# Optimization experiments

Measured on AMD Instinct MI355X. Metric: run time of the kernel, lower is better.

## Reference

```python
import jax, jax.numpy as jnp
import numpy as np

ETA = 1.0
BETA = 0.6
LN_EPS = 1e-5


def layer_norm(x, scale, bias):
    mu = x.mean(-1, keepdims=True)
    var = ((x - mu) ** 2).mean(-1, keepdims=True)
    return (x - mu) / jnp.sqrt(var + LN_EPS) * scale + bias


def setup_inputs() -> dict:
    B, N, S, C, D = 8, 2048, 16, 32, 128
    key = jax.random.key(0)
    ks = jax.random.split(key, 10)
    X_short = jax.random.normal(ks[0], (B, N, S, C), dtype=jnp.float32)
    # binary temporal validity mask (float, as multiplied in the original)
    mask_short = (jax.random.uniform(ks[1], (B, N, S)) > 0.3).astype(jnp.float32)
    A_stat = jax.random.uniform(ks[2], (N, N), dtype=jnp.float32)
    M_mask = jax.random.randint(ks[3], (N, N), 0, 2).astype(jnp.int32)
    M_mask = M_mask.at[jnp.arange(N), jnp.arange(N)].set(1)  # keep self-edges so no all-masked row
    node_reliab = jax.random.uniform(ks[4], (B, N), dtype=jnp.float32)
    # learned parameters (stored (in, out) so application is x @ W)
    W_proj = jax.random.normal(ks[5], (C, D), dtype=jnp.float32) / np.sqrt(C)
    Wq = jax.random.normal(ks[6], (D, D), dtype=jnp.float32) / np.sqrt(D)
    Wk = jax.random.normal(ks[7], (D, D), dtype=jnp.float32) / np.sqrt(D)
    W_lin = jax.random.normal(ks[8], (D, D), dtype=jnp.float32) / np.sqrt(D)
    ln1_scale = jnp.ones((D,), jnp.float32)
    ln1_bias = jnp.zeros((D,), jnp.float32)
    ln2_scale = jnp.ones((D,), jnp.float32)
    ln2_bias = jnp.zeros((D,), jnp.float32)
    return {
        "X_short": X_short, "mask_short": mask_short, "A_stat": A_stat,
        "M_mask": M_mask, "node_reliab": node_reliab,
        "W_proj": W_proj, "Wq": Wq, "Wk": Wk, "W_lin": W_lin,
        "ln1_scale": ln1_scale, "ln1_bias": ln1_bias,
        "ln2_scale": ln2_scale, "ln2_bias": ln2_bias,
    }


def reference(X_short, mask_short, A_stat, M_mask, node_reliab,
              W_proj, Wq, Wk, W_lin, ln1_scale, ln1_bias, ln2_scale, ln2_bias):
    D = W_proj.shape[1]
    # masked temporal mean pooling over S
    denom = jnp.maximum(mask_short.sum(axis=2, keepdims=True), 1.0)      # (B,N,1)
    x = (X_short * mask_short[..., None]).sum(axis=2) / denom            # (B,N,C)
    Hn = x @ W_proj                                                      # (B,N,D)
    # dynamic graph attention
    Q = Hn @ Wq
    K = Hn @ Wk
    logits = jnp.einsum('bnd,bmd->bnm', Q, K) / jnp.sqrt(jnp.float32(D))
    p = jnp.clip(A_stat, 1e-3, 1.0 - 1e-3)
    bias = jnp.log(p / (1.0 - p))                                        # logit
    logits = logits + ETA * bias[None]
    edge = (M_mask != 0)[None]                                           # (1,N,N)
    logits = jnp.where(edge, logits, -jnp.inf)
    Adyn = jax.nn.softmax(logits, axis=-1)                               # (B,N,N)
    # fuse with static adjacency, reliability scaling, mask, row-renormalize
    A_fuse = BETA * Adyn + (1.0 - BETA) * A_stat[None]
    r = jnp.clip(node_reliab, 0.0, 1.0)                                  # (B,N)
    A_fuse = A_fuse * r[:, :, None] * r[:, None, :]
    A_fuse = A_fuse * M_mask.astype(A_fuse.dtype)[None]
    A_fuse = A_fuse / (A_fuse.sum(axis=-1, keepdims=True) + 1e-8)
    # propagate: A @ H -> linear -> relu -> (dropout=eval identity) -> LN -> outer LN
    H = jnp.einsum('bnm,bmd->bnd', A_fuse, Hn)
    H = H @ W_lin
    H = layer_norm(jax.nn.relu(H), ln1_scale, ln1_bias)
    out = layer_norm(H, ln2_scale, ln2_bias)
    return out, A_fuse
```

## Files before the change

### kernel.cpp

```cpp
#include <hip/hip_runtime.h>
#include <math.h>

#define BB 8
#define NN 2048
#define SS 16
#define CC 32
#define DD 128

typedef unsigned short u16;
typedef __attribute__((ext_vector_type(8))) short bf16x8;
typedef __attribute__((ext_vector_type(4))) float f32x4;

__device__ inline u16 f2bf(float f) {
    union { float f; unsigned u; } c; c.f = f;
    unsigned r = c.u + 0x7fff + ((c.u >> 16) & 1);
    return (u16)(r >> 16);
}
__device__ inline float bf2f(u16 h) {
    union { unsigned u; float f; } c; c.u = ((unsigned)h) << 16;
    return c.f;
}
__device__ inline u16 f2h(float f) {
    union { _Float16 h; u16 u; } c; c.h = (_Float16)f;
    return c.u;
}
__device__ inline float h2f(u16 u) {
    union { _Float16 h; u16 v; } c; c.v = u;
    return (float)c.h;
}
__device__ inline float clamp01(float v) { return fminf(fmaxf(v, 0.f), 1.f); }

__global__ __launch_bounds__(256) void wcomb_kernel(const float* __restrict__ Wproj,
                                                    const float* __restrict__ Wq,
                                                    const float* __restrict__ Wk,
                                                    float* __restrict__ Wpq,
                                                    float* __restrict__ Wpk) {
    int g = blockIdx.x * 256 + threadIdx.x;
    int d = g & 127;
    int c = (g >> 7) & 31;
    int mat = g >> 12;
    const float* Wt = mat ? Wk : Wq;
    float acc = 0.f;
#pragma unroll 4
    for (int e = 0; e < DD; ++e)
        acc = fmaf(Wproj[c * DD + e], Wt[e * DD + d], acc);
    (mat ? Wpk : Wpq)[c * DD + d] = acc;
}

__global__ __launch_bounds__(256) void wlt_kernel(const float* __restrict__ Wl,
                                                  u16* __restrict__ WlT) {
    int g = blockIdx.x * 256 + threadIdx.x;
    int dp = g >> 7, d = g & 127;
    WlT[dp * DD + d] = f2bf(Wl[d * DD + dp]);
}

__global__ __launch_bounds__(256) void bias_prep_kernel(const float* __restrict__ Astat,
                                                        const int* __restrict__ Mm,
                                                        u16* __restrict__ lgh,
                                                        u16* __restrict__ am) {
    size_t g = ((size_t)blockIdx.x * 256 + threadIdx.x) * 4;
    float4 a4 = *(const float4*)&Astat[g];
    int4 m4 = *(const int4*)&Mm[g];
    float a[4] = {a4.x, a4.y, a4.z, a4.w};
    int mm[4] = {m4.x, m4.y, m4.z, m4.w};
    ushort4 lo, ao;
    u16 lg[4], ab[4];
#pragma unroll
    for (int j = 0; j < 4; ++j) {
        float p = fminf(fmaxf(a[j], 1e-3f), 1.f - 1e-3f);
        float l = __logf(p / (1.f - p));
        lg[j] = mm[j] ? f2h(l) : (u16)0xFC00;
        ab[j] = mm[j] ? f2bf(a[j]) : (u16)0;
    }
    lo.x = lg[0]; lo.y = lg[1]; lo.z = lg[2]; lo.w = lg[3];
    ao.x = ab[0]; ao.y = ab[1]; ao.z = ab[2]; ao.w = ab[3];
    *(ushort4*)&lgh[g] = lo;
    *(ushort4*)&am[g] = ao;
}

__global__ __launch_bounds__(256) void proj3_kernel(const float* __restrict__ X,
                                                    const float* __restrict__ Msk,
                                                    const float* __restrict__ Wproj,
                                                    const float* __restrict__ Wpq,
                                                    const float* __restrict__ Wpk,
                                                    u16* __restrict__ HnT,
                                                    u16* __restrict__ Qb,
                                                    u16* __restrict__ Kb) {
    __shared__ float wp[CC * DD], wq[CC * DD], wk[CC * DD];
    __shared__ float xs[CC * 36];
    int t = threadIdx.x;
    for (int i = t; i < CC * DD; i += 256) {
        wp[i] = Wproj[i];
        wq[i] = Wpq[i];
        wk[i] = Wpk[i];
    }
    int rbase = blockIdx.x * 32;
    {
        int row = t >> 3, cg = t & 7;
        const float* xrow = X + ((size_t)(rbase + row) * SS) * CC + cg * 4;
        const float* mrow = Msk + (size_t)(rbase + row) * SS;
        float4 acc = make_float4(0.f, 0.f, 0.f, 0.f);
        float msum = 0.f;
#pragma unroll
        for (int s = 0; s < SS; ++s) {
            float mv = mrow[s];
            float4 xv = *(const float4*)&xrow[s * CC];
            msum += mv;
            acc.x = fmaf(xv.x, mv, acc.x);
            acc.y = fmaf(xv.y, mv, acc.y);
            acc.z = fmaf(xv.z, mv, acc.z);
            acc.w = fmaf(xv.w, mv, acc.w);
        }
        float inv = 1.f / fmaxf(msum, 1.0f);
        xs[(cg * 4 + 0) * 36 + row] = acc.x * inv;
        xs[(cg * 4 + 1) * 36 + row] = acc.y * inv;
        xs[(cg * 4 + 2) * 36 + row] = acc.z * inv;
        xs[(cg * 4 + 3) * 36 + row] = acc.w * inv;
    }
    __syncthreads();

    int col = t & 127;
    int g = t >> 7;
    float ah[16], aq[16], ak[16];
#pragma unroll
    for (int i = 0; i < 16; ++i) { ah[i] = 0.f; aq[i] = 0.f; ak[i] = 0.f; }

#pragma unroll 4
    for (int k = 0; k < CC; ++k) {
        float wpv = wp[k * DD + col], wqv = wq[k * DD + col], wkv = wk[k * DD + col];
        const float4* xp = (const float4*)&xs[k * 36 + g * 16];
        float4 a0 = xp[0], a1 = xp[1], a2 = xp[2], a3 = xp[3];
        float xv[16] = {a0.x, a0.y, a0.z, a0.w, a1.x, a1.y, a1.z, a1.w,
                        a2.x, a2.y, a2.z, a2.w, a3.x, a3.y, a3.z, a3.w};
#pragma unroll
        for (int i = 0; i < 16; ++i) {
            ah[i] = fmaf(xv[i], wpv, ah[i]);
            aq[i] = fmaf(xv[i], wqv, aq[i]);
            ak[i] = fmaf(xv[i], wkv, ak[i]);
        }
    }
    const float scale = 0.08838834764831845f;
#pragma unroll
    for (int i = 0; i < 16; ++i) {
        size_t row = (size_t)(rbase + g * 16 + i);
        Qb[row * DD + col] = f2bf(aq[i] * scale);
        Kb[row * DD + col] = f2bf(ak[i]);
    }
    int b = rbase >> 11;
    int n0 = (rbase & (NN - 1)) + g * 16;
    u16* hp = HnT + (size_t)b * DD * NN + (size_t)col * NN + n0;
    unsigned pk[8];
#pragma unroll
    for (int i = 0; i < 8; ++i)
        pk[i] = (unsigned)f2bf(ah[2 * i]) | ((unsigned)f2bf(ah[2 * i + 1]) << 16);
    *(uint4*)&hp[0] = make_uint4(pk[0], pk[1], pk[2], pk[3]);
    *(uint4*)&hp[8] = make_uint4(pk[4], pk[5], pk[6], pk[7]);
}

#define LQT 136
__global__ __launch_bounds__(256) void stats_kernel(
        const u16* __restrict__ Qb, const u16* __restrict__ Kb,
        const u16* __restrict__ lgh, const u16* __restrict__ am,
        const float* __restrict__ rel,
        u16* __restrict__ Ebuf, float* __restrict__ part) {
    __shared__ u16 Qs[32 * LQT];
    __shared__ u16 Ks[128 * LQT];
    __shared__ float redE[128], redR[128], redA[128];
    int cs = blockIdx.x, rt = blockIdx.y, b = blockIdx.z;
    int R0 = rt * 32, C0 = cs * 512;
    int t = threadIdx.x;
    int lane = t & 63, w = t >> 6, q = lane >> 4, r16 = lane & 15;

    const u16* Qg = Qb + ((size_t)b * NN + R0) * DD;
#pragma unroll
    for (int rep = 0; rep < 2; ++rep) {
        int e = rep * 256 + t;
        int row = e >> 4, seg = e & 15;
        *(uint4*)&Qs[row * LQT + seg * 8] = *(const uint4*)&Qg[row * DD + seg * 8];
    }
    const u16* Kg = Kb + (size_t)b * NN * DD;
    float ER[2][4], LR[2][4], LA[2][4];
#pragma unroll
    for (int i = 0; i < 2; ++i)
#pragma unroll
        for (int r = 0; r < 4; ++r) { ER[i][r] = 0.f; LR[i][r] = 0.f; LA[i][r] = 0.f; }

    for (int ct = 0; ct < 4; ++ct) {
        __syncthreads();
#pragma unroll
        for (int rep = 0; rep < 8; ++rep) {
            int e = rep * 256 + t;
            int colr = e >> 4, seg = e & 15;
            *(uint4*)&Ks[colr * LQT + seg * 8] =
                *(const uint4*)&Kg[(size_t)(C0 + ct * 128 + colr) * DD + seg * 8];
        }
        __syncthreads();
        f32x4 acc[2][2];
#pragma unroll
        for (int i = 0; i < 2; ++i)
#pragma unroll
            for (int j = 0; j < 2; ++j)
                acc[i][j] = (f32x4){0.f, 0.f, 0.f, 0.f};
#pragma unroll
        for (int ksp = 0; ksp < 4; ++ksp) {
            int ko = ksp * 32 + q * 8;
            bf16x8 a0 = *(const bf16x8*)&Qs[r16 * LQT + ko];
            bf16x8 a1 = *(const bf16x8*)&Qs[(16 + r16) * LQT + ko];
            bf16x8 b0 = *(const bf16x8*)&Ks[(w * 32 + r16) * LQT + ko];
            bf16x8 b1 = *(const bf16x8*)&Ks[(w * 32 + 16 + r16) * LQT + ko];
            acc[0][0] = __builtin_amdgcn_mfma_f32_16x16x32_bf16(a0, b0, acc[0][0], 0, 0, 0);
            acc[0][1] = __builtin_amdgcn_mfma_f32_16x16x32_bf16(a0, b1, acc[0][1], 0, 0, 0);
            acc[1][0] = __builtin_amdgcn_mfma_f32_16x16x32_bf16(a1, b0, acc[1][0], 0, 0, 0);
            acc[1][1] = __builtin_amdgcn_mfma_f32_16x16x32_bf16(a1, b1, acc[1][1], 0, 0, 0);
        }
        int m0 = C0 + ct * 128 + w * 32;
        float rm0 = clamp01(rel[b * NN + m0 + r16]);
        float rm1 = clamp01(rel[b * NN + m0 + 16 + r16]);
#pragma unroll
        for (int i = 0; i < 2; ++i)
#pragma unroll
            for (int r = 0; r < 4; ++r) {
                int n = R0 + i * 16 + q * 4 + r;
                const u16* lrow = lgh + (size_t)n * NN + m0;
                const u16* arow = am + (size_t)n * NN + m0;
                float lg0 = h2f(lrow[r16]), lg1 = h2f(lrow[16 + r16]);
                float a0 = bf2f(arow[r16]), a1 = bf2f(arow[16 + r16]);
                u16 eb0 = f2bf(__expf(acc[i][0][r] + lg0));
                u16 eb1 = f2bf(__expf(acc[i][1][r] + lg1));
                size_t o = ((size_t)b * NN + n) * NN + m0;
                Ebuf[o + r16] = eb0;
                Ebuf[o + 16 + r16] = eb1;
                float e0 = bf2f(eb0), e1 = bf2f(eb1);
                ER[i][r] += e0 + e1;
                LR[i][r] = fmaf(e0, rm0, fmaf(e1, rm1, LR[i][r]));
                LA[i][r] = fmaf(a0, rm0, fmaf(a1, rm1, LA[i][r]));
            }
    }
#pragma unroll
    for (int i = 0; i < 2; ++i)
#pragma unroll
        for (int r = 0; r < 4; ++r) {
            float e = ER[i][r], lr = LR[i][r], la = LA[i][r];
#pragma unroll
            for (int off = 1; off < 16; off <<= 1) {
                e += __shfl_xor(e, off);
                lr += __shfl_xor(lr, off);
                la += __shfl_xor(la, off);
            }
            if (r16 == 0) {
                int row = i * 16 + q * 4 + r;
                redE[w * 32 + row] = e;
                redR[w * 32 + row] = lr;
                redA[w * 32 + row] = la;
            }
        }
    __syncthreads();
    if (t < 32) {
        float es = redE[t] + redE[32 + t] + redE[64 + t] + redE[96 + t];
        float lr = redR[t] + redR[32 + t] + redR[64 + t] + redR[96 + t];
        float la = redA[t] + redA[32 + t] + redA[64 + t] + redA[96 + t];
        float* p = part + ((size_t)((b * 64 + rt) * 4 + cs)) * 96;
        p[t] = es;
        p[32 + t] = lr;
        p[64 + t] = la;
    }
}

#define LPT 72
#define LWT 136
__global__ __launch_bounds__(256) void prop_kernel(
        const u16* __restrict__ Ebuf, const u16* __restrict__ am,
        const float* __restrict__ part, const float* __restrict__ rel,
        const u16* __restrict__ HnT, const u16* __restrict__ WlT,
        const float* __restrict__ s1, const float* __restrict__ b1,
        const float* __restrict__ s2, const float* __restrict__ b2,
        float* __restrict__ Af, float* __restrict__ out) {
    __shared__ union {
        struct { u16 As[32 * LPT]; u16 Bs[128 * LPT]; } ab;
        struct { u16 Ws[128 * LWT]; u16 Hs[32 * LWT]; } fin;
    } sm;
    __shared__ float redS[128], redQ[128];
    __shared__ float2 MV[32];
    __shared__ float2 cfs[32];
    int rt = blockIdx.x, b = blockIdx.y;
    int R0 = rt * 32;
    int t = threadIdx.x;
    int lane = t & 63, w = t >> 6, q = lane >> 4, r16 = lane & 15;
    int srow = t >> 3, sseg = t & 7;

    if (t < 32) {
        const float* p = part + ((size_t)((b * 64 + rt) * 4)) * 96;
        float es = 0.f, lr = 0.f, la = 0.f;
#pragma unroll
        for (int cs = 0; cs < 4; ++cs) {
            es += p[cs * 96 + t];
            lr += p[cs * 96 + 32 + t];
            la += p[cs * 96 + 64 + t];
        }
        float rn = clamp01(rel[b * NN + R0 + t]);
        float inv = 1.f / es;
        float fsum = rn * (0.6f * lr * inv + 0.4f * la);
        float nrm = 1.f / (fsum + 1e-8f);
        cfs[t] = make_float2(0.6f * inv * rn * nrm, 0.4f * rn * nrm);
    }
    __syncthreads();

    int n = R0 + srow;
    float2 cf = cfs[srow];
    const u16* Eg = Ebuf + ((size_t)b * NN + n) * NN;
    const u16* ag = am + (size_t)n * NN;
    const float* rg = rel + b * NN;
    const u16* Bg = HnT + (size_t)b * DD * NN;
    float* Afg = Af + ((size_t)b * NN + n) * NN;

    f32x4 acc[2][2];
#pragma unroll
    for (int i = 0; i < 2; ++i)
#pragma unroll
        for (int j = 0; j < 2; ++j)
            acc[i][j] = (f32x4){0.f, 0.f, 0.f, 0.f};

    for (int kc = 0; kc < NN; kc += 64) {
        __syncthreads();
        {
            int m = kc + sseg * 8;
            uint4 ev = *(const uint4*)&Eg[m];
            uint4 av = *(const uint4*)&ag[m];
            float4 r0 = *(const float4*)&rg[m];
            float4 r1 = *(const float4*)&rg[m + 4];
            unsigned eu[4] = {ev.x, ev.y, ev.z, ev.w};
            unsigned au[4] = {av.x, av.y, av.z, av.w};
            float rm[8] = {clamp01(r0.x), clamp01(r0.y), clamp01(r0.z), clamp01(r0.w),
                           clamp01(r1.x), clamp01(r1.y), clamp01(r1.z), clamp01(r1.w)};
            float v[8];
            unsigned pk[4];
#pragma unroll
            for (int j = 0; j < 4; ++j) {
                float e0 = bf2f((u16)(eu[j] & 0xffff));
                float e1 = bf2f((u16)(eu[j] >> 16));
                float a0 = bf2f((u16)(au[j] & 0xffff));
                float a1 = bf2f((u16)(au[j] >> 16));
                v[2 * j] = rm[2 * j] * fmaf(e0, cf.x, a0 * cf.y);
                v[2 * j + 1] = rm[2 * j + 1] * fmaf(e1, cf.x, a1 * cf.y);
                pk[j] = (unsigned)f2bf(v[2 * j]) | ((unsigned)f2bf(v[2 * j + 1]) << 16);
            }
            *(float4*)&Afg[m] = make_float4(v[0], v[1], v[2], v[3]);
            *(float4*)&Afg[m + 4] = make_float4(v[4], v[5], v[6], v[7]);
            *(uint4*)&sm.ab.As[srow * LPT + sseg * 8] = make_uint4(pk[0], pk[1], pk[2], pk[3]);
        }
#pragma unroll
        for (int rep = 0; rep < 4; ++rep) {
            int e = rep * 256 + t;
            int d = e >> 3, sg = e & 7;
            *(uint4*)&sm.ab.Bs[d * LPT + sg * 8] =
                *(const uint4*)&Bg[(size_t)d * NN + kc + sg * 8];
        }
        __syncthreads();
#pragma unroll
        for (int kst = 0; kst < 2; ++kst) {
            int ko = kst * 32 + q * 8;
            bf16x8 a0 = *(const bf16x8*)&sm.ab.As[r16 * LPT + ko];
            bf16x8 a1 = *(const bf16x8*)&sm.ab.As[(16 + r16) * LPT + ko];
            bf16x8 b0 = *(const bf16x8*)&sm.ab.Bs[(w * 32 + r16) * LPT + ko];
            bf16x8 b1v = *(const bf16x8*)&sm.ab.Bs[(w * 32 + 16 + r16) * LPT + ko];
            acc[0][0] = __builtin_amdgcn_mfma_f32_16x16x32_bf16(a0, b0, acc[0][0], 0, 0, 0);
            acc[0][1] = __builtin_amdgcn_mfma_f32_16x16x32_bf16(a0, b1v, acc[0][1], 0, 0, 0);
            acc[1][0] = __builtin_amdgcn_mfma_f32_16x16x32_bf16(a1, b0, acc[1][0], 0, 0, 0);
            acc[1][1] = __builtin_amdgcn_mfma_f32_16x16x32_bf16(a1, b1v, acc[1][1], 0, 0, 0);
        }
    }

    __syncthreads();
#pragma unroll
    for (int rep = 0; rep < 8; ++rep) {
        int e = rep * 256 + t;
        int dp = e >> 4, seg = e & 15;
        *(uint4*)&sm.fin.Ws[dp * LWT + seg * 8] = *(const uint4*)&WlT[dp * DD + seg * 8];
    }
#pragma unroll
    for (int i = 0; i < 2; ++i)
#pragma unroll
        for (int j = 0; j < 2; ++j)
#pragma unroll
            for (int r = 0; r < 4; ++r)
                sm.fin.Hs[(i * 16 + q * 4 + r) * LWT + w * 32 + j * 16 + r16] =
                    f2bf(acc[i][j][r]);
    __syncthreads();

    f32x4 c2[2][2];
#pragma unroll
    for (int i = 0; i < 2; ++i)
#pragma unroll
        for (int j = 0; j < 2; ++j)
            c2[i][j] = (f32x4){0.f, 0.f, 0.f, 0.f};
#pragma unroll
    for (int ksp = 0; ksp < 4; ++ksp) {
        int ko = ksp * 32 + q * 8;
        bf16x8 a0 = *(const bf16x8*)&sm.fin.Hs[r16 * LWT + ko];
        bf16x8 a1 = *(const bf16x8*)&sm.fin.Hs[(16 + r16) * LWT + ko];
        bf16x8 b0 = *(const bf16x8*)&sm.fin.Ws[(w * 32 + r16) * LWT + ko];
        bf16x8 b1v = *(const bf16x8*)&sm.fin.Ws[(w * 32 + 16 + r16) * LWT + ko];
        c2[0][0] = __builtin_amdgcn_mfma_f32_16x16x32_bf16(a0, b0, c2[0][0], 0, 0, 0);
        c2[0][1] = __builtin_amdgcn_mfma_f32_16x16x32_bf16(a0, b1v, c2[0][1], 0, 0, 0);
        c2[1][0] = __builtin_amdgcn_mfma_f32_16x16x32_bf16(a1, b0, c2[1][0], 0, 0, 0);
        c2[1][1] = __builtin_amdgcn_mfma_f32_16x16x32_bf16(a1, b1v, c2[1][1], 0, 0, 0);
    }
    float v[2][2][4];
#pragma unroll
    for (int i = 0; i < 2; ++i)
#pragma unroll
        for (int j = 0; j < 2; ++j)
#pragma unroll
            for (int r = 0; r < 4; ++r)
                v[i][j][r] = fmaxf(c2[i][j][r], 0.f);

    int c0 = w * 32 + r16, c1 = w * 32 + 16 + r16;
    float s1c0 = s1[c0], s1c1 = s1[c1], b1c0 = b1[c0], b1c1 = b1[c1];
    float s2c0 = s2[c0], s2c1 = s2[c1], b2c0 = b2[c0], b2c1 = b2[c1];

#pragma unroll
    for (int i = 0; i < 2; ++i)
#pragma unroll
        for (int r = 0; r < 4; ++r) {
            float s = v[i][0][r] + v[i][1][r];
            float qq = v[i][0][r] * v[i][0][r] + v[i][1][r] * v[i][1][r];
#pragma unroll
            for (int off = 1; off < 16; off <<= 1) {
                s += __shfl_xor(s, off);
                qq += __shfl_xor(qq, off);
            }
            if (r16 == 0) {
                int row = i * 16 + q * 4 + r;
                redS[w * 32 + row] = s;
                redQ[w * 32 + row] = qq;
            }
        }
    __syncthreads();
    if (t < 32) {
        float s = redS[t] + redS[32 + t] + redS[64 + t] + redS[96 + t];
        float qq = redQ[t] + redQ[32 + t] + redQ[64 + t] + redQ[96 + t];
        float mu = s * (1.f / 128.f);
        float var = qq * (1.f / 128.f) - mu * mu;
        MV[t] = make_float2(mu, 1.f / sqrtf(var + 1e-5f));
    }
    __syncthreads();
    float y[2][2][4];
#pragma unroll
    for (int i = 0; i < 2; ++i)
#pragma unroll
        for (int r = 0; r < 4; ++r) {
            float2 mv = MV[i * 16 + q * 4 + r];
            y[i][0][r] = (v[i][0][r] - mv.x) * mv.y * s1c0 + b1c0;
            y[i][1][r] = (v[i][1][r] - mv.x) * mv.y * s1c1 + b1c1;
        }
    __syncthreads();
#pragma unroll
    for (int i = 0; i < 2; ++i)
#pragma unroll
        for (int r = 0; r < 4; ++r) {
            float s = y[i][0][r] + y[i][1][r];
            float qq = y[i][0][r] * y[i][0][r] + y[i][1][r] * y[i][1][r];
#pragma unroll
            for (int off = 1; off < 16; off <<= 1) {
                s += __shfl_xor(s, off);
                qq += __shfl_xor(qq, off);
            }
            if (r16 == 0) {
                int row = i * 16 + q * 4 + r;
                redS[w * 32 + row] = s;
                redQ[w * 32 + row] = qq;
            }
        }
    __syncthreads();
    if (t < 32) {
        float s = redS[t] + redS[32 + t] + redS[64 + t] + redS[96 + t];
        float qq = redQ[t] + redQ[32 + t] + redQ[64 + t] + redQ[96 + t];
        float mu = s * (1.f / 128.f);
        float var = qq * (1.f / 128.f) - mu * mu;
        MV[t] = make_float2(mu, 1.f / sqrtf(var + 1e-5f));
    }
    __syncthreads();
#pragma unroll
    for (int i = 0; i < 2; ++i)
#pragma unroll
        for (int r = 0; r < 4; ++r) {
            float2 mv = MV[i * 16 + q * 4 + r];
            size_t o = ((size_t)b * NN + R0 + i * 16 + q * 4 + r) * DD;
            out[o + c0] = (y[i][0][r] - mv.x) * mv.y * s2c0 + b2c0;
            out[o + c1] = (y[i][1][r] - mv.x) * mv.y * s2c1 + b2c1;
        }
}

extern "C" void kernel_launch(void* const* d_in, const int* in_sizes, int n_in,
                              void* d_out, int out_size, void* d_ws, size_t ws_size,
                              hipStream_t stream) {
    const float* X = (const float*)d_in[0];
    const float* Msk = (const float*)d_in[1];
    const float* Astat = (const float*)d_in[2];
    const int* Mm = (const int*)d_in[3];
    const float* rel = (const float*)d_in[4];
    const float* Wproj = (const float*)d_in[5];
    const float* Wq = (const float*)d_in[6];
    const float* Wk = (const float*)d_in[7];
    const float* Wlin = (const float*)d_in[8];
    const float* s1 = (const float*)d_in[9];
    const float* b1 = (const float*)d_in[10];
    const float* s2 = (const float*)d_in[11];
    const float* b2 = (const float*)d_in[12];

    float* outMain = (float*)d_out;
    float* Afuse = outMain + (size_t)BB * NN * DD;

    float* w_ = (float*)d_ws;
    float* Wpq = w_;
    float* Wpk = w_ + 4096;
    u16* WlT = (u16*)(w_ + 8192);
    u16* Qb = (u16*)(w_ + 16384);
    u16* Kb = (u16*)(w_ + 1064960);
    u16* HnT = (u16*)(w_ + 2113536);
    u16* lgh = (u16*)(w_ + 3162112);
    u16* am = (u16*)(w_ + 5259264);
    u16* Ebuf = (u16*)(w_ + 7356416);
    float* part = w_ + 24133632;

    wcomb_kernel<<<dim3(32), dim3(256), 0, stream>>>(Wproj, Wq, Wk, Wpq, Wpk);
    wlt_kernel<<<dim3(64), dim3(256), 0, stream>>>(Wlin, WlT);
    bias_prep_kernel<<<dim3(4096), dim3(256), 0, stream>>>(Astat, Mm, lgh, am);
    proj3_kernel<<<dim3(512), dim3(256), 0, stream>>>(X, Msk, Wproj, Wpq, Wpk, HnT, Qb, Kb);

    stats_kernel<<<dim3(4, 64, 8), dim3(256), 0, stream>>>(
        Qb, Kb, lgh, am, rel, Ebuf, part);
    prop_kernel<<<dim3(64, 8), dim3(256), 0, stream>>>(
        Ebuf, am, part, rel, HnT, WlT, s1, b1, s2, b2, Afuse, outMain);
}
```

Baseline: 358.1 us.

## Merge prep kernels and give prop kernel 512 threads with register prefetch

The three small preparation kernels (weight combine, W_lin transpose, bias/mask prep) become one launch, with the weight work handled by two extra blocks. The propagation kernel goes from 256 to 512 threads, so each wave now owns a 16x32 output tile instead of 32x32. It also prefetches the next K-chunk of E, mask, reliability and HnT into registers while the current chunk is consumed from shared memory. The aim is to hide global-load latency in the bandwidth-bound A_fuse write/GEMM loop and cut launch overhead. The cost is more threads competing for the same shared memory and a few more registers per thread.

```diff
diff --git a/kernel.cpp b/kernel.cpp
--- a/kernel.cpp
+++ b/kernel.cpp
@@ -30,52 +30,55 @@
 }
 __device__ inline float clamp01(float v) { return fminf(fmaxf(v, 0.f), 1.f); }
 
-__global__ __launch_bounds__(256) void wcomb_kernel(const float* __restrict__ Wproj,
-                                                    const float* __restrict__ Wq,
-                                                    const float* __restrict__ Wk,
-                                                    float* __restrict__ Wpq,
-                                                    float* __restrict__ Wpk) {
-    int g = blockIdx.x * 256 + threadIdx.x;
-    int d = g & 127;
-    int c = (g >> 7) & 31;
-    int mat = g >> 12;
-    const float* Wt = mat ? Wk : Wq;
-    float acc = 0.f;
+__global__ __launch_bounds__(256) void prep_kernel(const float* __restrict__ Astat,
+                                                   const int* __restrict__ Mm,
+                                                   const float* __restrict__ Wproj,
+                                                   const float* __restrict__ Wq,
+                                                   const float* __restrict__ Wk,
+                                                   const float* __restrict__ Wl,
+                                                   u16* __restrict__ lgh,
+                                                   u16* __restrict__ am,
+                                                   float* __restrict__ Wpq,
+                                                   float* __restrict__ Wpk,
+                                                   u16* __restrict__ WlT) {
+    int bx = blockIdx.x;
+    if (bx < 4096) {
+        size_t g = ((size_t)bx * 256 + threadIdx.x) * 4;
+        float4 a4 = *(const float4*)&Astat[g];
+        int4 m4 = *(const int4*)&Mm[g];
+        float a[4] = {a4.x, a4.y, a4.z, a4.w};
+        int mm[4] = {m4.x, m4.y, m4.z, m4.w};
+        ushort4 lo, ao;
+        u16 lg[4], ab[4];
+#pragma unroll
+        for (int j = 0; j < 4; ++j) {
+            float p = fminf(fmaxf(a[j], 1e-3f), 1.f - 1e-3f);
+            float l = __logf(p / (1.f - p));
+            lg[j] = mm[j] ? f2h(l) : (u16)0xFC00;
+            ab[j] = mm[j] ? f2bf(a[j]) : (u16)0;
+        }
+        lo.x = lg[0]; lo.y = lg[1]; lo.z = lg[2]; lo.w = lg[3];
+        ao.x = ab[0]; ao.y = ab[1]; ao.z = ab[2]; ao.w = ab[3];
+        *(ushort4*)&lgh[g] = lo;
+        *(ushort4*)&am[g] = ao;
+    } else if (bx == 4096) {
+        for (int i = threadIdx.x; i < 8192; i += 256) {
+            int d = i & 127;
+            int c = (i >> 7) & 31;
+            int mat = i >> 12;
+            const float* Wt = mat ? Wk : Wq;
+            float acc = 0.f;
 #pragma unroll 4
-    for (int e = 0; e < DD; ++e)
-        acc = fmaf(Wproj[c * DD + e], Wt[e * DD + d], acc);
-    (mat ? Wpk : Wpq)[c * DD + d] = acc;
-}
-
-__global__ __launch_bounds__(256) void wlt_kernel(const float* __restrict__ Wl,
-                                                  u16* __restrict__ WlT) {
-    int g = blockIdx.x * 256 + threadIdx.x;
-    int dp = g >> 7, d = g & 127;
-    WlT[dp * DD + d] = f2bf(Wl[d * DD + dp]);
-}
-
-__global__ __launch_bounds__(256) void bias_prep_kernel(const float* __restrict__ Astat,
-                                                        const int* __restrict__ Mm,
-                                                        u16* __restrict__ lgh,
-                                                        u16* __restrict__ am) {
-    size_t g = ((size_t)blockIdx.x * 256 + threadIdx.x) * 4;
-    float4 a4 = *(const float4*)&Astat[g];
-    int4 m4 = *(const int4*)&Mm[g];
-    float a[4] = {a4.x, a4.y, a4.z, a4.w};
-    int mm[4] = {m4.x, m4.y, m4.z, m4.w};
-    ushort4 lo, ao;
-    u16 lg[4], ab[4];
-#pragma unroll
-    for (int j = 0; j < 4; ++j) {
-        float p = fminf(fmaxf(a[j], 1e-3f), 1.f - 1e-3f);
-        float l = __logf(p / (1.f - p));
-        lg[j] = mm[j] ? f2h(l) : (u16)0xFC00;
-        ab[j] = mm[j] ? f2bf(a[j]) : (u16)0;
-    }
-    lo.x = lg[0]; lo.y = lg[1]; lo.z = lg[2]; lo.w = lg[3];
-    ao.x = ab[0]; ao.y = ab[1]; ao.z = ab[2]; ao.w = ab[3];
-    *(ushort4*)&lgh[g] = lo;
-    *(ushort4*)&am[g] = ao;
+            for (int e = 0; e < DD; ++e)
+                acc = fmaf(Wproj[c * DD + e], Wt[e * DD + d], acc);
+            (mat ? Wpk : Wpq)[c * DD + d] = acc;
+        }
+    } else {
+        for (int i = threadIdx.x; i < 16384; i += 256) {
+            int dp = i >> 7, d = i & 127;
+            WlT[dp * DD + d] = f2bf(Wl[d * DD + dp]);
+        }
+    }
 }
 
 __global__ __launch_bounds__(256) void proj3_kernel(const float* __restrict__ X,
@@ -268,7 +271,7 @@
 
 #define LPT 72
 #define LWT 136
-__global__ __launch_bounds__(256) void prop_kernel(
+__global__ __launch_bounds__(512) void prop_kernel(
         const u16* __restrict__ Ebuf, const u16* __restrict__ am,
         const float* __restrict__ part, const float* __restrict__ rel,
         const u16* __restrict__ HnT, const u16* __restrict__ WlT,
@@ -286,7 +289,8 @@
     int R0 = rt * 32;
     int t = threadIdx.x;
     int lane = t & 63, w = t >> 6, q = lane >> 4, r16 = lane & 15;
-    int srow = t >> 3, sseg = t & 7;
+    int wr = (w >> 2) * 16;
+    int wc = (w & 3) * 32;
 
     if (t < 32) {
         const float* p = part + ((size_t)((b * 64 + rt) * 4)) * 96;
@@ -305,136 +309,120 @@
     }
     __syncthreads();
 
-    int n = R0 + srow;
-    float2 cf = cfs[srow];
-    const u16* Eg = Ebuf + ((size_t)b * NN + n) * NN;
-    const u16* ag = am + (size_t)n * NN;
+    int arow = t >> 4, ac = (t & 15) * 4;
+    float2 cf = cfs[arow];
+    const u16* Eg = Ebuf + ((size_t)b * NN + R0 + arow) * NN;
+    const u16* ag = am + (size_t)(R0 + arow) * NN;
     const float* rg = rel + b * NN;
     const u16* Bg = HnT + (size_t)b * DD * NN;
-    float* Afg = Af + ((size_t)b * NN + n) * NN;
-
-    f32x4 acc[2][2];
-#pragma unroll
-    for (int i = 0; i < 2; ++i)
-#pragma unroll
-        for (int j = 0; j < 2; ++j)
-            acc[i][j] = (f32x4){0.f, 0.f, 0.f, 0.f};
+    float* Afg = Af + ((size_t)b * NN + R0 + arow) * NN;
+
+    int bd0 = t >> 3, bs0 = (t & 7) * 8;
+    int bd1 = (512 + t) >> 3, bs1 = bs0;
+
+    f32x4 acc[2];
+    acc[0] = (f32x4){0.f, 0.f, 0.f, 0.f};
+    acc[1] = (f32x4){0.f, 0.f, 0.f, 0.f};
+
+    uint2 pe = *(const uint2*)&Eg[ac];
+    uint2 pa = *(const uint2*)&ag[ac];
+    float4 pr = *(const float4*)&rg[ac];
+    uint4 pb0 = *(const uint4*)&Bg[(size_t)bd0 * NN + bs0];
+    uint4 pb1 = *(const uint4*)&Bg[(size_t)bd1 * NN + bs1];
 
     for (int kc = 0; kc < NN; kc += 64) {
         __syncthreads();
         {
-            int m = kc + sseg * 8;
-            uint4 ev = *(const uint4*)&Eg[m];
-            uint4 av = *(const uint4*)&ag[m];
-            float4 r0 = *(const float4*)&rg[m];
-            float4 r1 = *(const float4*)&rg[m + 4];
-            unsigned eu[4] = {ev.x, ev.y, ev.z, ev.w};
-            unsigned au[4] = {av.x, av.y, av.z, av.w};
-            float rm[8] = {clamp01(r0.x), clamp01(r0.y), clamp01(r0.z), clamp01(r0.w),
-                           clamp01(r1.x), clamp01(r1.y), clamp01(r1.z), clamp01(r1.w)};
-            float v[8];
-            unsigned pk[4];
-#pragma unroll
-            for (int j = 0; j < 4; ++j) {
-                float e0 = bf2f((u16)(eu[j] & 0xffff));
-                float e1 = bf2f((u16)(eu[j] >> 16));
-                float a0 = bf2f((u16)(au[j] & 0xffff));
-                float a1 = bf2f((u16)(au[j] >> 16));
-                v[2 * j] = rm[2 * j] * fmaf(e0, cf.x, a0 * cf.y);
-                v[2 * j + 1] = rm[2 * j + 1] * fmaf(e1, cf.x, a1 * cf.y);
-                pk[j] = (unsigned)f2bf(v[2 * j]) | ((unsigned)f2bf(v[2 * j + 1]) << 16);
-            }
-            *(float4*)&Afg[m] = make_float4(v[0], v[1], v[2], v[3]);
-            *(float4*)&Afg[m + 4] = make_float4(v[4], v[5], v[6], v[7]);
-            *(uint4*)&sm.ab.As[srow * LPT + sseg * 8] = make_uint4(pk[0], pk[1], pk[2], pk[3]);
-        }
-#pragma unroll
-        for (int rep = 0; rep < 4; ++rep) {
-            int e = rep * 256 + t;
-            int d = e >> 3, sg = e & 7;
-            *(uint4*)&sm.ab.Bs[d * LPT + sg * 8] =
-                *(const uint4*)&Bg[(size_t)d * NN + kc + sg * 8];
+            float e0 = bf2f((u16)(pe.x & 0xffff)), e1 = bf2f((u16)(pe.x >> 16));
+            float e2 = bf2f((u16)(pe.y & 0xffff)), e3 = bf2f((u16)(pe.y >> 16));
+            float a0 = bf2f((u16)(pa.x & 0xffff)), a1 = bf2f((u16)(pa.x >> 16));
+            float a2 = bf2f((u16)(pa.y & 0xffff)), a3 = bf2f((u16)(pa.y >> 16));
+            float r0 = clamp01(pr.x), r1 = clamp01(pr.y);
+            float r2 = clamp01(pr.z), r3 = clamp01(pr.w);
+            float v0 = r0 * fmaf(e0, cf.x, a0 * cf.y);
+            float v1 = r1 * fmaf(e1, cf.x, a1 * cf.y);
+            float v2 = r2 * fmaf(e2, cf.x, a2 * cf.y);
+            float v3 = r3 * fmaf(e3, cf.x, a3 * cf.y);
+            *(float4*)&Afg[kc + ac] = make_float4(v0, v1, v2, v3);
+            unsigned pk0 = (unsigned)f2bf(v0) | ((unsigned)f2bf(v1) << 16);
+            unsigned pk1 = (unsigned)f2bf(v2) | ((unsigned)f2bf(v3) << 16);
+            *(uint2*)&sm.ab.As[arow * LPT + ac] = make_uint2(pk0, pk1);
+        }
+        *(uint4*)&sm.ab.Bs[bd0 * LPT + bs0] = pb0;
+        *(uint4*)&sm.ab.Bs[bd1 * LPT + bs1] = pb1;
+        if (kc + 64 < NN) {
+            int kn = kc + 64;
+            pe = *(const uint2*)&Eg[kn + ac];
+            pa = *(const uint2*)&ag[kn + ac];
+            pr = *(const float4*)&rg[kn + ac];
+            pb0 = *(const uint4*)&Bg[(size_t)bd0 * NN + kn + bs0];
+            pb1 = *(const uint4*)&Bg[(size_t)bd1 * NN + kn + bs1];
         }
         __syncthreads();
 #pragma unroll
         for (int kst = 0; kst < 2; ++kst) {
             int ko = kst * 32 + q * 8;
-            bf16x8 a0 = *(const bf16x8*)&sm.ab.As[r16 * LPT + ko];
-            bf16x8 a1 = *(const bf16x8*)&sm.ab.As[(16 + r16) * LPT + ko];
-            bf16x8 b0 = *(const bf16x8*)&sm.ab.Bs[(w * 32 + r16) * LPT + ko];
-            bf16x8 b1v = *(const bf16x8*)&sm.ab.Bs[(w * 32 + 16 + r16) * LPT + ko];
-            acc[0][0] = __builtin_amdgcn_mfma_f32_16x16x32_bf16(a0, b0, acc[0][0], 0, 0, 0);
-            acc[0][1] = __builtin_amdgcn_mfma_f32_16x16x32_bf16(a0, b1v, acc[0][1], 0, 0, 0);
-            acc[1][0] = __builtin_amdgcn_mfma_f32_16x16x32_bf16(a1, b0, acc[1][0], 0, 0, 0);
-            acc[1][1] = __builtin_amdgcn_mfma_f32_16x16x32_bf16(a1, b1v, acc[1][1], 0, 0, 0);
-        }
-    }
-
-    __syncthreads();
-#pragma unroll
-    for (int rep = 0; rep < 8; ++rep) {
-        int e = rep * 256 + t;
+            bf16x8 a0 = *(const bf16x8*)&sm.ab.As[(wr + r16) * LPT + ko];
+            bf16x8 b0 = *(const bf16x8*)&sm.ab.Bs[(wc + r16) * LPT + ko];
+            bf16x8 b1v = *(const bf16x8*)&sm.ab.Bs[(wc + 16 + r16) * LPT + ko];
+            acc[0] = __builtin_amdgcn_mfma_f32_16x16x32_bf16(a0, b0, acc[0], 0, 0, 0);
+            acc[1] = __builtin_amdgcn_mfma_f32_16x16x32_bf16(a0, b1v, acc[1], 0, 0, 0);
+        }
+    }
+
+    __syncthreads();
+#pragma unroll
+    for (int rep = 0; rep < 4; ++rep) {
+        int e = rep * 512 + t;
         int dp = e >> 4, seg = e & 15;
         *(uint4*)&sm.fin.Ws[dp * LWT + seg * 8] = *(const uint4*)&WlT[dp * DD + seg * 8];
     }
 #pragma unroll
-    for (int i = 0; i < 2; ++i)
-#pragma unroll
-        for (int j = 0; j < 2; ++j)
-#pragma unroll
-            for (int r = 0; r < 4; ++r)
-                sm.fin.Hs[(i * 16 + q * 4 + r) * LWT + w * 32 + j * 16 + r16] =
-                    f2bf(acc[i][j][r]);
-    __syncthreads();
-
-    f32x4 c2[2][2];
-#pragma unroll
-    for (int i = 0; i < 2; ++i)
-#pragma unroll
-        for (int j = 0; j < 2; ++j)
-            c2[i][j] = (f32x4){0.f, 0.f, 0.f, 0.f};
+    for (int j = 0; j < 2; ++j)
+#pragma unroll
+        for (int r = 0; r < 4; ++r)
+            sm.fin.Hs[(wr + q * 4 + r) * LWT + wc + j * 16 + r16] = f2bf(acc[j][r]);
+    __syncthreads();
+
+    f32x4 c2[2];
+    c2[0] = (f32x4){0.f, 0.f, 0.f, 0.f};
+    c2[1] = (f32x4){0.f, 0.f, 0.f, 0.f};
 #pragma unroll
     for (int ksp = 0; ksp < 4; ++ksp) {
         int ko = ksp * 32 + q * 8;
-        bf16x8 a0 = *(const bf16x8*)&sm.fin.Hs[r16 * LWT + ko];
-        bf16x8 a1 = *(const bf16x8*)&sm.fin.Hs[(16 + r16) * LWT + ko];
-        bf16x8 b0 = *(const bf16x8*)&sm.fin.Ws[(w * 32 + r16) * LWT + ko];
-        bf16x8 b1v = *(const bf16x8*)&sm.fin.Ws[(w * 32 + 16 + r16) * LWT + ko];
-        c2[0][0] = __builtin_amdgcn_mfma_f32_16x16x32_bf16(a0, b0, c2[0][0], 0, 0, 0);
-        c2[0][1] = __builtin_amdgcn_mfma_f32_16x16x32_bf16(a0, b1v, c2[0][1], 0, 0, 0);
-        c2[1][0] = __builtin_amdgcn_mfma_f32_16x16x32_bf16(a1, b0, c2[1][0], 0, 0, 0);
-        c2[1][1] = __builtin_amdgcn_mfma_f32_16x16x32_bf16(a1, b1v, c2[1][1], 0, 0, 0);
-    }
-    float v[2][2][4];
-#pragma unroll
-    for (int i = 0; i < 2; ++i)
-#pragma unroll
-        for (int j = 0; j < 2; ++j)
-#pragma unroll
-            for (int r = 0; r < 4; ++r)
-                v[i][j][r] = fmaxf(c2[i][j][r], 0.f);
-
-    int c0 = w * 32 + r16, c1 = w * 32 + 16 + r16;
+        bf16x8 a0 = *(const bf16x8*)&sm.fin.Hs[(wr + r16) * LWT + ko];
+        bf16x8 b0 = *(const bf16x8*)&sm.fin.Ws[(wc + r16) * LWT + ko];
+        bf16x8 b1v = *(const bf16x8*)&sm.fin.Ws[(wc + 16 + r16) * LWT + ko];
+        c2[0] = __builtin_amdgcn_mfma_f32_16x16x32_bf16(a0, b0, c2[0], 0, 0, 0);
+        c2[1] = __builtin_amdgcn_mfma_f32_16x16x32_bf16(a0, b1v, c2[1], 0, 0, 0);
+    }
+    float v[2][4];
+#pragma unroll
+    for (int j = 0; j < 2; ++j)
+#pragma unroll
+        for (int r = 0; r < 4; ++r)
+            v[j][r] = fmaxf(c2[j][r], 0.f);
+
+    int c0 = wc + r16, c1 = wc + 16 + r16;
     float s1c0 = s1[c0], s1c1 = s1[c1], b1c0 = b1[c0], b1c1 = b1[c1];
     float s2c0 = s2[c0], s2c1 = s2[c1], b2c0 = b2[c0], b2c1 = b2[c1];
-
-#pragma unroll
-    for (int i = 0; i < 2; ++i)
-#pragma unroll
-        for (int r = 0; r < 4; ++r) {
-            float s = v[i][0][r] + v[i][1][r];
-            float qq = v[i][0][r] * v[i][0][r] + v[i][1][r] * v[i][1][r];
-#pragma unroll
-            for (int off = 1; off < 16; off <<= 1) {
-                s += __shfl_xor(s, off);
-                qq += __shfl_xor(qq, off);
-            }
-            if (r16 == 0) {
-                int row = i * 16 + q * 4 + r;
-                redS[w * 32 + row] = s;
-                redQ[w * 32 + row] = qq;
-            }
-        }
+    int g4 = (w & 3) * 32;
+
+#pragma unroll
+    for (int r = 0; r < 4; ++r) {
+        float s = v[0][r] + v[1][r];
+        float qq = v[0][r] * v[0][r] + v[1][r] * v[1][r];
+#pragma unroll
+        for (int off = 1; off < 16; off <<= 1) {
+            s += __shfl_xor(s, off);
+            qq += __shfl_xor(qq, off);
+        }
+        if (r16 == 0) {
+            int row = wr + q * 4 + r;
+            redS[g4 + row] = s;
+            redQ[g4 + row] = qq;
+        }
+    }
     __syncthreads();
     if (t < 32) {
         float s = redS[t] + redS[32 + t] + redS[64 + t] + redS[96 + t];
@@ -444,33 +432,29 @@
         MV[t] = make_float2(mu, 1.f / sqrtf(var + 1e-5f));
     }
     __syncthreads();
-    float y[2][2][4];
-#pragma unroll
-    for (int i = 0; i < 2; ++i)
-#pragma unroll
-        for (int r = 0; r < 4; ++r) {
-            float2 mv = MV[i * 16 + q * 4 + r];
-            y[i][0][r] = (v[i][0][r] - mv.x) * mv.y * s1c0 + b1c0;
-            y[i][1][r] = (v[i][1][r] - mv.x) * mv.y * s1c1 + b1c1;
-        }
-    __syncthreads();
-#pragma unroll
-    for (int i = 0; i < 2; ++i)
-#pragma unroll
-        for (int r = 0; r < 4; ++r) {
-            float s = y[i][0][r] + y[i][1][r];
-            float qq = y[i][0][r] * y[i][0][r] + y[i][1][r] * y[i][1][r];
-#pragma unroll
-            for (int off = 1; off < 16; off <<= 1) {
-                s += __shfl_xor(s, off);
-                qq += __shfl_xor(qq, off);
-            }
-            if (r16 == 0) {
-                int row = i * 16 + q * 4 + r;
-                redS[w * 32 + row] = s;
-                redQ[w * 32 + row] = qq;
-            }
-        }
+    float y[2][4];
+#pragma unroll
+    for (int r = 0; r < 4; ++r) {
+        float2 mv = MV[wr + q * 4 + r];
+        y[0][r] = (v[0][r] - mv.x) * mv.y * s1c0 + b1c0;
+        y[1][r] = (v[1][r] - mv.x) * mv.y * s1c1 + b1c1;
+    }
+    __syncthreads();
+#pragma unroll
+    for (int r = 0; r < 4; ++r) {
+        float s = y[0][r] + y[1][r];
+        float qq = y[0][r] * y[0][r] + y[1][r] * y[1][r];
+#pragma unroll
+        for (int off = 1; off < 16; off <<= 1) {
+            s += __shfl_xor(s, off);
+            qq += __shfl_xor(qq, off);
+        }
+        if (r16 == 0) {
+            int row = wr + q * 4 + r;
+            redS[g4 + row] = s;
+            redQ[g4 + row] = qq;
+        }
+    }
     __syncthreads();
     if (t < 32) {
         float s = redS[t] + redS[32 + t] + redS[64 + t] + redS[96 + t];
@@ -481,14 +465,12 @@
     }
     __syncthreads();
 #pragma unroll
-    for (int i = 0; i < 2; ++i)
-#pragma unroll
-        for (int r = 0; r < 4; ++r) {
-            float2 mv = MV[i * 16 + q * 4 + r];
-            size_t o = ((size_t)b * NN + R0 + i * 16 + q * 4 + r) * DD;
-            out[o + c0] = (y[i][0][r] - mv.x) * mv.y * s2c0 + b2c0;
-            out[o + c1] = (y[i][1][r] - mv.x) * mv.y * s2c1 + b2c1;
-        }
+    for (int r = 0; r < 4; ++r) {
+        float2 mv = MV[wr + q * 4 + r];
+        size_t o = ((size_t)b * NN + R0 + wr + q * 4 + r) * DD;
+        out[o + c0] = (y[0][r] - mv.x) * mv.y * s2c0 + b2c0;
+        out[o + c1] = (y[1][r] - mv.x) * mv.y * s2c1 + b2c1;
+    }
 }
 
 extern "C" void kernel_launch(void* const* d_in, const int* in_sizes, int n_in,
@@ -523,13 +505,12 @@
     u16* Ebuf = (u16*)(w_ + 7356416);
     float* part = w_ + 24133632;
 
-    wcomb_kernel<<<dim3(32), dim3(256), 0, stream>>>(Wproj, Wq, Wk, Wpq, Wpk);
-    wlt_kernel<<<dim3(64), dim3(256), 0, stream>>>(Wlin, WlT);
-    bias_prep_kernel<<<dim3(4096), dim3(256), 0, stream>>>(Astat, Mm, lgh, am);
+    prep_kernel<<<dim3(4098), dim3(256), 0, stream>>>(
+        Astat, Mm, Wproj, Wq, Wk, Wlin, lgh, am, Wpq, Wpk, WlT);
     proj3_kernel<<<dim3(512), dim3(256), 0, stream>>>(X, Msk, Wproj, Wpq, Wpk, HnT, Qb, Kb);
 
     stats_kernel<<<dim3(4, 64, 8), dim3(256), 0, stream>>>(
         Qb, Kb, lgh, am, rel, Ebuf, part);
-    prop_kernel<<<dim3(64, 8), dim3(256), 0, stream>>>(
+    prop_kernel<<<dim3(64, 8), dim3(512), 0, stream>>>(
         Ebuf, am, part, rel, HnT, WlT, s1, b1, s2, b2, Afuse, outMain);
 }
```

Measured after the change: 489.7 us. 1.37x slower.
